# Kernel optimization log

Measured on AMD Instinct MI355X. Metric: run time of the kernel, lower is better.

Reference implementation:

```python
import jax, jax.numpy as jnp
import numpy as np

NUM_USER = 100000
NUM_ITEM = 50000
N = NUM_USER + NUM_ITEM          # total nodes
D = 64                            # dim_latent
E = 2400000                       # nnz of sparse graph
NUM_LAYER = 3


def setup_inputs() -> dict:
    key = jax.random.key(0)
    k1, k2, k3, k4, k5 = jax.random.split(key, 5)
    user_emb = jax.random.normal(k1, (NUM_USER, D), dtype=jnp.float32)
    item_emb = jax.random.normal(k2, (NUM_ITEM, D), dtype=jnp.float32)
    graph_rows = jax.random.randint(k3, (E,), 0, N, dtype=jnp.int32)
    graph_cols = jax.random.randint(k4, (E,), 0, N, dtype=jnp.int32)
    # normalized-adjacency-like small positive values
    graph_vals = jax.random.uniform(k5, (E,), dtype=jnp.float32) * 0.01
    return {
        "user_emb": user_emb,
        "item_emb": item_emb,
        "graph_vals": graph_vals,
        "graph_rows": graph_rows,
        "graph_cols": graph_cols,
    }


def _spmm(vals, rows, cols, x):
    # sparse [N,N] @ dense [N,D] via gather + segment_sum
    gathered = vals[:, None] * x[cols]            # [E, D]
    return jax.ops.segment_sum(gathered, rows, num_segments=N)  # [N, D]


def reference(user_emb, item_emb, graph_vals, graph_rows, graph_cols):
    all_emb = jnp.concatenate([user_emb, item_emb], axis=0)   # [N, D]
    acc = all_emb
    emb = all_emb
    for _ in range(NUM_LAYER):
        emb = _spmm(graph_vals, graph_rows, graph_cols, emb)
        acc = acc + emb
    light_out = acc / jnp.float32(NUM_LAYER + 1)              # mean over layer dim
    return (light_out, user_emb, item_emb)
```

## Files before the change

### kernel.cpp

```cpp
#include <hip/hip_runtime.h>


#define NUM_USER 100000
#define NUM_ITEM 50000
#define NTOT     150000
#define DIM      64
#define NEDGE    2400000
#define ND       (NTOT * DIM)

#define RPB    256
#define NB     586
#define CAP    4736
#define CHUNK  4096
#define NCHUNK 586
#define EPT    16
#define CVTB   1024

typedef float v2f __attribute__((ext_vector_type(2)));

static __device__ __forceinline__ unsigned pk_fp8x4(float a, float b, float c, float d) {
    int p = 0;
    p = __builtin_amdgcn_cvt_pk_fp8_f32(a, b, p, false);
    p = __builtin_amdgcn_cvt_pk_fp8_f32(c, d, p, true);
    return (unsigned)p;
}
static __device__ __forceinline__ unsigned char f2fp8(float a) {
    return (unsigned char)(__builtin_amdgcn_cvt_pk_fp8_f32(a, 0.f, 0, false) & 0xFF);
}
static __device__ __forceinline__ float fp8lo2f(unsigned w) {
    const v2f t = __builtin_amdgcn_cvt_pk_f32_fp8((int)w, false);
    return t[0];
}

__global__ __launch_bounds__(256) void phaseA_kernel(
    const int*   __restrict__ rows,
    const int*   __restrict__ cols,
    const float* __restrict__ vals,
    int*            __restrict__ cursor,
    unsigned*       __restrict__ crG,
    unsigned short* __restrict__ vbG,
    const float*    __restrict__ user,
    const float*    __restrict__ item,
    unsigned*       __restrict__ xq)
{
    __shared__ unsigned       s_cr[CHUNK];
    __shared__ unsigned short s_vb[CHUNK];
    __shared__ unsigned short s_bk[CHUNK];
    __shared__ int s_hist[NB];
    __shared__ int s_scan[NB];
    __shared__ int s_dst[NB];
    __shared__ int s_cur[NB];
    __shared__ int s_part[256];

    if (blockIdx.x >= NCHUNK) {
        const int nvec  = ND / 4;
        const int userv = NUM_USER * DIM / 4;
        for (int i = (blockIdx.x - NCHUNK) * 256 + threadIdx.x; i < nvec;
             i += CVTB * 256) {
            const float4 v = (i < userv) ? ((const float4*)user)[i]
                                         : ((const float4*)item)[i - userv];
            xq[i] = pk_fp8x4(v.x * 16.f, v.y * 16.f, v.z * 16.f, v.w * 16.f);
        }
        return;
    }

    const int t    = threadIdx.x;
    const int base = blockIdx.x * CHUNK;
    const int n    = min(CHUNK, NEDGE - base);

    for (int i = t; i < NB; i += 256) s_hist[i] = 0;
    __syncthreads();

    int            mrow[EPT];
    unsigned       mcol[EPT];
    unsigned short mvb[EPT];
#pragma unroll
    for (int k = 0; k < EPT; ++k) {
        const int i = t + k * 256;
        if (i < n) {
            const int e = base + i;
            mrow[k] = rows[e];
            mcol[k] = (unsigned)cols[e];
            mvb[k]  = f2fp8(vals[e] * 64.f);
            atomicAdd(&s_hist[mrow[k] >> 8], 1);
        } else mrow[k] = -1;
    }
    __syncthreads();

    int loc[3]; int ssum = 0;
#pragma unroll
    for (int k = 0; k < 3; ++k) {
        const int i = t * 3 + k;
        loc[k] = (i < NB) ? s_hist[i] : 0;
        ssum += loc[k];
    }
    s_part[t] = ssum;
    __syncthreads();
    for (int o = 1; o < 256; o <<= 1) {
        const int v = (t >= o) ? s_part[t - o] : 0;
        __syncthreads();
        s_part[t] += v;
        __syncthreads();
    }
    int run = s_part[t] - ssum;
#pragma unroll
    for (int k = 0; k < 3; ++k) {
        const int i = t * 3 + k;
        if (i < NB) { s_scan[i] = run; run += loc[k]; }
    }
    __syncthreads();

    for (int i = t; i < NB; i += 256) {
        const int c = s_hist[i];
        s_dst[i] = i * CAP + (c ? atomicAdd(&cursor[i], c) : 0);
        s_cur[i] = s_scan[i];
    }
    __syncthreads();

#pragma unroll
    for (int k = 0; k < EPT; ++k) {
        if (mrow[k] >= 0) {
            const int b   = mrow[k] >> 8;
            const int pos = atomicAdd(&s_cur[b], 1);
            s_cr[pos] = mcol[k] | ((unsigned)(mrow[k] & 255) << 18);
            s_vb[pos] = mvb[k];
            s_bk[pos] = (unsigned short)b;
        }
    }
    __syncthreads();

    for (int p = t; p < n; p += 256) {
        const int b = s_bk[p];
        const int g = s_dst[b] + (p - s_scan[b]);
        crG[g] = s_cr[p];
        vbG[g] = s_vb[p];
    }
}

__global__ __launch_bounds__(256) void phaseB_kernel(
    const int*      __restrict__ cursor,
    unsigned*       __restrict__ crG,
    unsigned short* __restrict__ vbG,
    int*            __restrict__ rowbeg,
    int*            __restrict__ rowend)
{
    __shared__ unsigned       s_cr[CAP];
    __shared__ unsigned short s_vb[CAP];
    __shared__ unsigned short s_idx[CAP];
    __shared__ int s_hist[RPB];
    __shared__ int s_scan[RPB];
    __shared__ int s_cur[RPB];

    const int b = blockIdx.x, t = threadIdx.x;
    const int gbase = b * CAP;
    const int cnt = cursor[b];

    s_hist[t] = 0;
    __syncthreads();
    for (int p = t; p < cnt; p += 256) {
        const unsigned cr = crG[gbase + p];
        s_cr[p] = cr;
        s_vb[p] = vbG[gbase + p];
        atomicAdd(&s_hist[cr >> 18], 1);
    }
    __syncthreads();

    const int h = s_hist[t];
    s_scan[t] = h;
    __syncthreads();
    for (int o = 1; o < 256; o <<= 1) {
        const int v = (t >= o) ? s_scan[t - o] : 0;
        __syncthreads();
        s_scan[t] += v;
        __syncthreads();
    }
    const int excl = s_scan[t] - h;
    s_cur[t] = excl;
    __syncthreads();

    for (int p = t; p < cnt; p += 256) {
        const int r   = s_cr[p] >> 18;
        const int pos = atomicAdd(&s_cur[r], 1);
        s_idx[pos] = (unsigned short)p;
    }
    __syncthreads();

    for (int p = t; p < cnt; p += 256) {
        const int i = s_idx[p];
        crG[gbase + p] = ((s_cr[i] & 0x3FFFFu) << 8) | (unsigned)(s_vb[i] & 0xFFu);
    }
    const int row = b * RPB + t;
    if (row < NTOT) {
        rowbeg[row] = gbase + excl;
        rowend[row] = gbase + excl + h;
    }
}

template<int MODE>
__global__ __launch_bounds__(256) void spmm_pull(
    const int*            __restrict__ rowbeg,
    const int*            __restrict__ rowend,
    const unsigned*       __restrict__ cv,
    const unsigned char*  __restrict__ xq,
    unsigned*             __restrict__ destq,
    float*                __restrict__ acc,
    const float*          __restrict__ user,
    const float*          __restrict__ item,
    float*                __restrict__ out)
{
    const int r    = (blockIdx.x * 256 + threadIdx.x) >> 6;
    const int lane = threadIdx.x & 63;
    const int g    = lane >> 3;
    const int l    = lane & 7;

    const int beg = __builtin_amdgcn_readfirstlane(rowbeg[r]);
    const int end = __builtin_amdgcn_readfirstlane(rowend[r]);

    v2f a0 = {0.f,0.f}, a1 = {0.f,0.f}, a2 = {0.f,0.f}, a3 = {0.f,0.f};
    for (int k = beg + g; k < end; k += 16) {
        const bool h1 = (k + 8) < end;
        const int  kb = h1 ? k + 8 : k;
        const unsigned ca = cv[k];
        unsigned cb = cv[kb];
        cb = h1 ? cb : (cb & ~0xFFu);

        const float va = fp8lo2f(ca);
        const float vb = fp8lo2f(cb);

        const unsigned offA = ((ca & ~0xFFu) >> 2) + (l << 3);
        const unsigned offB = ((cb & ~0xFFu) >> 2) + (l << 3);
        const uint2 wa = *reinterpret_cast<const uint2*>(xq + offA);
        const uint2 wb = *reinterpret_cast<const uint2*>(xq + offB);

        const v2f va2 = {va, va}, vb2 = {vb, vb};
        a0 += va2 * __builtin_amdgcn_cvt_pk_f32_fp8((int)wa.x, false);
        a1 += va2 * __builtin_amdgcn_cvt_pk_f32_fp8((int)wa.x, true);
        a2 += va2 * __builtin_amdgcn_cvt_pk_f32_fp8((int)wa.y, false);
        a3 += va2 * __builtin_amdgcn_cvt_pk_f32_fp8((int)wa.y, true);
        a0 += vb2 * __builtin_amdgcn_cvt_pk_f32_fp8((int)wb.x, false);
        a1 += vb2 * __builtin_amdgcn_cvt_pk_f32_fp8((int)wb.x, true);
        a2 += vb2 * __builtin_amdgcn_cvt_pk_f32_fp8((int)wb.y, false);
        a3 += vb2 * __builtin_amdgcn_cvt_pk_f32_fp8((int)wb.y, true);
    }

    float f0 = a0[0], f1 = a0[1], f2 = a1[0], f3 = a1[1];
    float f4 = a2[0], f5 = a2[1], f6 = a3[0], f7 = a3[1];
#define RED(x) x += __shfl_xor(x, 8); x += __shfl_xor(x, 16); x += __shfl_xor(x, 32);
    RED(f0) RED(f1) RED(f2) RED(f3) RED(f4) RED(f5) RED(f6) RED(f7)
#undef RED
    const float s = 1.f / 1024.f;
    f0 *= s; f1 *= s; f2 *= s; f3 *= s; f4 *= s; f5 *= s; f6 *= s; f7 *= s;

    if (g == 0) {
        const int o = r * DIM + (l << 3);
        if (MODE == 0) {
            *reinterpret_cast<float4*>(acc + o)     = make_float4(f0, f1, f2, f3);
            *reinterpret_cast<float4*>(acc + o + 4) = make_float4(f4, f5, f6, f7);
        } else if (MODE == 1) {
            float4 x0 = *reinterpret_cast<float4*>(acc + o);
            float4 x1 = *reinterpret_cast<float4*>(acc + o + 4);
            x0.x += f0; x0.y += f1; x0.z += f2; x0.w += f3;
            x1.x += f4; x1.y += f5; x1.z += f6; x1.w += f7;
            *reinterpret_cast<float4*>(acc + o)     = x0;
            *reinterpret_cast<float4*>(acc + o + 4) = x1;
        } else {
            const float* aep = (r < NUM_USER)
                ? user + (size_t)r * DIM + (l << 3)
                : item + (size_t)(r - NUM_USER) * DIM + (l << 3);
            const float4 e0 = *reinterpret_cast<const float4*>(aep);
            const float4 e1 = *reinterpret_cast<const float4*>(aep + 4);
            const float4 x0 = *reinterpret_cast<const float4*>(acc + o);
            const float4 x1 = *reinterpret_cast<const float4*>(acc + o + 4);
            float4 lo0, lo1;
            lo0.x = (x0.x + f0 + e0.x) * 0.25f;
            lo0.y = (x0.y + f1 + e0.y) * 0.25f;
            lo0.z = (x0.z + f2 + e0.z) * 0.25f;
            lo0.w = (x0.w + f3 + e0.w) * 0.25f;
            lo1.x = (x1.x + f4 + e1.x) * 0.25f;
            lo1.y = (x1.y + f5 + e1.y) * 0.25f;
            lo1.z = (x1.z + f6 + e1.z) * 0.25f;
            lo1.w = (x1.w + f7 + e1.w) * 0.25f;
            *reinterpret_cast<float4*>(out + o)          = lo0;
            *reinterpret_cast<float4*>(out + o + 4)      = lo1;
            *reinterpret_cast<float4*>(out + ND + o)     = e0;
            *reinterpret_cast<float4*>(out + ND + o + 4) = e1;
        }
        if (MODE == 0 || MODE == 1) {
            uint2 pk;
            pk.x = pk_fp8x4(f0 * 16.f, f1 * 16.f, f2 * 16.f, f3 * 16.f);
            pk.y = pk_fp8x4(f4 * 16.f, f5 * 16.f, f6 * 16.f, f7 * 16.f);
            *reinterpret_cast<uint2*>(destq + (r << 4) + (l << 1)) = pk;
        }
    }
}


__global__ __launch_bounds__(256) void spmm_atomic(
    const float* __restrict__ vals, const int* __restrict__ rows,
    const int* __restrict__ cols, const float* __restrict__ x0,
    const float* __restrict__ x1, int split, float* __restrict__ out)
{
    const int lane = threadIdx.x & 63;
    const long wave   = ((long)blockIdx.x * blockDim.x + threadIdx.x) >> 6;
    const long nwaves = ((long)gridDim.x * blockDim.x) >> 6;
    for (long e = wave; e < NEDGE; e += nwaves) {
        const int   r = rows[e];
        const int   c = cols[e];
        const float v = vals[e];
        const float xv = (c < split) ? x0[(long)c * DIM + lane]
                                     : x1[(long)(c - split) * DIM + lane];
        atomicAdd(&out[(long)r * DIM + lane], v * xv);
    }
}

__global__ __launch_bounds__(256) void add2_kernel(
    const float* __restrict__ a, const float* __restrict__ b,
    float* __restrict__ acc)
{
    const int nvec = ND / 4;
    for (int i = blockIdx.x * blockDim.x + threadIdx.x; i < nvec;
         i += gridDim.x * blockDim.x) {
        const float4 av = ((const float4*)a)[i];
        const float4 bv = ((const float4*)b)[i];
        float4 o;
        o.x = av.x + bv.x; o.y = av.y + bv.y;
        o.z = av.z + bv.z; o.w = av.w + bv.w;
        ((float4*)acc)[i] = o;
    }
}

__global__ __launch_bounds__(256) void finalize3_kernel(
    const float* __restrict__ user, const float* __restrict__ item,
    float* __restrict__ out)
{
    const int nvec  = ND / 4;
    const int userv = NUM_USER * DIM / 4;
    for (int i = blockIdx.x * blockDim.x + threadIdx.x; i < nvec;
         i += gridDim.x * blockDim.x) {
        const float4 ae = (i < userv) ? ((const float4*)user)[i]
                                      : ((const float4*)item)[i - userv];
        const float4 ac = ((const float4*)out)[i];
        const float4 e3 = ((const float4*)(out + ND))[i];
        float4 lo;
        lo.x = (ae.x + ac.x + e3.x) * 0.25f;
        lo.y = (ae.y + ac.y + e3.y) * 0.25f;
        lo.z = (ae.z + ac.z + e3.z) * 0.25f;
        lo.w = (ae.w + ac.w + e3.w) * 0.25f;
        ((float4*)out)[i] = lo;
        ((float4*)(out + ND))[i] = ae;
    }
}


extern "C" void kernel_launch(void* const* d_in, const int* in_sizes, int n_in,
                              void* d_out, int out_size, void* d_ws, size_t ws_size,
                              hipStream_t stream) {
    const float* user = (const float*)d_in[0];
    const float* item = (const float*)d_in[1];
    const float* vals = (const float*)d_in[2];
    const int*   rows = (const int*)d_in[3];
    const int*   cols = (const int*)d_in[4];

    float* out = (float*)d_out;
    float* acc = out;

    char* w = (char*)d_ws;
    unsigned char* xq0 = (unsigned char*)w;
    unsigned char* xq1 = xq0 + ND;
    unsigned*      crG = (unsigned*)(xq1 + ND);
    int*   rowbeg = (int*)(crG + (size_t)NB * CAP);
    int*   rowend = rowbeg + NTOT;
    int*   cursor = rowend + NTOT;
    unsigned short* vbG = (unsigned short*)(cursor + NB);
    const size_t ws_need = (size_t)ND * 2 + (size_t)NB * CAP * 6
                         + (size_t)(2 * NTOT + NB) * 4 + 64;

    if (ws_size >= ws_need) {
        hipMemsetAsync(cursor, 0, (size_t)NB * 4, stream);
        phaseA_kernel<<<NCHUNK + CVTB, 256, 0, stream>>>(
            rows, cols, vals, cursor, crG, vbG, user, item, (unsigned*)xq0);
        phaseB_kernel<<<NB, 256, 0, stream>>>(cursor, crG, vbG, rowbeg, rowend);

        const int spmm_blocks = NTOT / 4;
        spmm_pull<0><<<spmm_blocks, 256, 0, stream>>>(rowbeg, rowend, crG,
            xq0, (unsigned*)xq1, acc, nullptr, nullptr, nullptr);
        spmm_pull<1><<<spmm_blocks, 256, 0, stream>>>(rowbeg, rowend, crG,
            xq1, (unsigned*)xq0, acc, nullptr, nullptr, nullptr);
        spmm_pull<2><<<spmm_blocks, 256, 0, stream>>>(rowbeg, rowend, crG,
            xq0, nullptr, acc, user, item, out);
    } else {
        float* bufA = (float*)d_ws;
        float* out1 = out + ND;
        const size_t nd_bytes = (size_t)ND * sizeof(float);
        hipMemsetAsync(out1, 0, nd_bytes, stream);
        spmm_atomic<<<2048, 256, 0, stream>>>(vals, rows, cols, user, item, NUM_USER, out1);
        hipMemsetAsync(bufA, 0, nd_bytes, stream);
        spmm_atomic<<<2048, 256, 0, stream>>>(vals, rows, cols, out1, out1, NTOT, bufA);
        add2_kernel<<<2048, 256, 0, stream>>>(out1, bufA, acc);
        hipMemsetAsync(out1, 0, nd_bytes, stream);
        spmm_atomic<<<2048, 256, 0, stream>>>(vals, rows, cols, bufA, bufA, NTOT, out1);
        finalize3_kernel<<<2048, 256, 0, stream>>>(user, item, out);
    }
}
```

Before: 233.6 us.

## Process row cohorts per wave in column-segment order for cache locality

Phase B now sorts edges within each row by a 3-bit column-range key, so every row gets 8 segment ranges. The SpMM kernel assigns 37 consecutive rows to each wave and walks those rows segment by segment. This keeps the gathered fp8 source rows inside a narrow column window at any moment, which is meant to improve L2/MALL hit rates. In exchange each wave holds 37 register accumulators, each lane gathers only 2 bytes per edge, the grid is much smaller, and the loop has more index overhead.

Measured after the change: 740.2 us. +216.8%, slower.

```diff
diff --git a/kernel.cpp b/kernel.cpp
--- a/kernel.cpp
+++ b/kernel.cpp
@@ -16,6 +16,11 @@
 #define EPT    16
 #define CVTB   1024
 
+#define NSEG   5
+#define NKEY   2048
+#define RW     37
+#define COHORT_BLOCKS 1014
+
 typedef float v2f __attribute__((ext_vector_type(2)));
 
 static __device__ __forceinline__ unsigned pk_fp8x4(float a, float b, float c, float d) {
@@ -26,10 +31,6 @@
 }
 static __device__ __forceinline__ unsigned char f2fp8(float a) {
     return (unsigned char)(__builtin_amdgcn_cvt_pk_fp8_f32(a, 0.f, 0, false) & 0xFF);
-}
-static __device__ __forceinline__ float fp8lo2f(unsigned w) {
-    const v2f t = __builtin_amdgcn_cvt_pk_f32_fp8((int)w, false);
-    return t[0];
 }
 
 __global__ __launch_bounds__(256) void phaseA_kernel(
@@ -140,47 +141,56 @@
 __global__ __launch_bounds__(256) void phaseB_kernel(
     const int*      __restrict__ cursor,
     unsigned*       __restrict__ crG,
-    unsigned short* __restrict__ vbG,
-    int*            __restrict__ rowbeg,
-    int*            __restrict__ rowend)
+    const unsigned short* __restrict__ vbG,
+    int2*           __restrict__ segbe)
 {
     __shared__ unsigned       s_cr[CAP];
     __shared__ unsigned short s_vb[CAP];
     __shared__ unsigned short s_idx[CAP];
-    __shared__ int s_hist[RPB];
-    __shared__ int s_scan[RPB];
-    __shared__ int s_cur[RPB];
+    __shared__ int s_hist[NKEY];
+    __shared__ int s_cur[NKEY];
+    __shared__ int s_part[256];
 
     const int b = blockIdx.x, t = threadIdx.x;
     const int gbase = b * CAP;
     const int cnt = cursor[b];
 
-    s_hist[t] = 0;
+    for (int i = t; i < NKEY; i += 256) s_hist[i] = 0;
     __syncthreads();
     for (int p = t; p < cnt; p += 256) {
         const unsigned cr = crG[gbase + p];
         s_cr[p] = cr;
         s_vb[p] = vbG[gbase + p];
-        atomicAdd(&s_hist[cr >> 18], 1);
-    }
-    __syncthreads();
-
-    const int h = s_hist[t];
-    s_scan[t] = h;
+        const int key = (int)(((cr >> 18) << 3) | ((cr >> 15) & 7u));
+        atomicAdd(&s_hist[key], 1);
+    }
+    __syncthreads();
+
+    int loc[8]; int ssum = 0;
+#pragma unroll
+    for (int j = 0; j < 8; ++j) { loc[j] = s_hist[t * 8 + j]; ssum += loc[j]; }
+    s_part[t] = ssum;
     __syncthreads();
     for (int o = 1; o < 256; o <<= 1) {
-        const int v = (t >= o) ? s_scan[t - o] : 0;
+        const int v = (t >= o) ? s_part[t - o] : 0;
         __syncthreads();
-        s_scan[t] += v;
+        s_part[t] += v;
         __syncthreads();
     }
-    const int excl = s_scan[t] - h;
-    s_cur[t] = excl;
+    int run = s_part[t] - ssum;
+    __syncthreads();
+#pragma unroll
+    for (int j = 0; j < 8; ++j) {
+        s_hist[t * 8 + j] = run;
+        s_cur[t * 8 + j]  = run;
+        run += loc[j];
+    }
     __syncthreads();
 
     for (int p = t; p < cnt; p += 256) {
-        const int r   = s_cr[p] >> 18;
-        const int pos = atomicAdd(&s_cur[r], 1);
+        const unsigned cr = s_cr[p];
+        const int key = (int)(((cr >> 18) << 3) | ((cr >> 15) & 7u));
+        const int pos = atomicAdd(&s_cur[key], 1);
         s_idx[pos] = (unsigned short)p;
     }
     __syncthreads();
@@ -189,107 +199,98 @@
         const int i = s_idx[p];
         crG[gbase + p] = ((s_cr[i] & 0x3FFFFu) << 8) | (unsigned)(s_vb[i] & 0xFFu);
     }
-    const int row = b * RPB + t;
-    if (row < NTOT) {
-        rowbeg[row] = gbase + excl;
-        rowend[row] = gbase + excl + h;
+    __syncthreads();
+
+    for (int i = t; i < NKEY; i += 256) {
+        const int row = b * RPB + (i >> 3);
+        if (row < NTOT)
+            segbe[(row << 3) | (i & 7)] =
+                make_int2(gbase + s_hist[i], gbase + s_cur[i]);
     }
 }
 
 template<int MODE>
-__global__ __launch_bounds__(256) void spmm_pull(
-    const int*            __restrict__ rowbeg,
-    const int*            __restrict__ rowend,
+__global__ __launch_bounds__(256, 4) void spmm_cohort(
+    const int2*           __restrict__ segbe,
     const unsigned*       __restrict__ cv,
     const unsigned char*  __restrict__ xq,
-    unsigned*             __restrict__ destq,
+    unsigned char*        __restrict__ destq,
     float*                __restrict__ acc,
     const float*          __restrict__ user,
     const float*          __restrict__ item,
     float*                __restrict__ out)
 {
-    const int r    = (blockIdx.x * 256 + threadIdx.x) >> 6;
+    const int wave = ((blockIdx.x << 8) + threadIdx.x) >> 6;
     const int lane = threadIdx.x & 63;
-    const int g    = lane >> 3;
-    const int l    = lane & 7;
-
-    const int beg = __builtin_amdgcn_readfirstlane(rowbeg[r]);
-    const int end = __builtin_amdgcn_readfirstlane(rowend[r]);
-
-    v2f a0 = {0.f,0.f}, a1 = {0.f,0.f}, a2 = {0.f,0.f}, a3 = {0.f,0.f};
-    for (int k = beg + g; k < end; k += 16) {
-        const bool h1 = (k + 8) < end;
-        const int  kb = h1 ? k + 8 : k;
-        const unsigned ca = cv[k];
-        unsigned cb = cv[kb];
-        cb = h1 ? cb : (cb & ~0xFFu);
-
-        const float va = fp8lo2f(ca);
-        const float vb = fp8lo2f(cb);
-
-        const unsigned offA = ((ca & ~0xFFu) >> 2) + (l << 3);
-        const unsigned offB = ((cb & ~0xFFu) >> 2) + (l << 3);
-        const uint2 wa = *reinterpret_cast<const uint2*>(xq + offA);
-        const uint2 wb = *reinterpret_cast<const uint2*>(xq + offB);
-
-        const v2f va2 = {va, va}, vb2 = {vb, vb};
-        a0 += va2 * __builtin_amdgcn_cvt_pk_f32_fp8((int)wa.x, false);
-        a1 += va2 * __builtin_amdgcn_cvt_pk_f32_fp8((int)wa.x, true);
-        a2 += va2 * __builtin_amdgcn_cvt_pk_f32_fp8((int)wa.y, false);
-        a3 += va2 * __builtin_amdgcn_cvt_pk_f32_fp8((int)wa.y, true);
-        a0 += vb2 * __builtin_amdgcn_cvt_pk_f32_fp8((int)wb.x, false);
-        a1 += vb2 * __builtin_amdgcn_cvt_pk_f32_fp8((int)wb.x, true);
-        a2 += vb2 * __builtin_amdgcn_cvt_pk_f32_fp8((int)wb.y, false);
-        a3 += vb2 * __builtin_amdgcn_cvt_pk_f32_fp8((int)wb.y, true);
-    }
-
-    float f0 = a0[0], f1 = a0[1], f2 = a1[0], f3 = a1[1];
-    float f4 = a2[0], f5 = a2[1], f6 = a3[0], f7 = a3[1];
-#define RED(x) x += __shfl_xor(x, 8); x += __shfl_xor(x, 16); x += __shfl_xor(x, 32);
-    RED(f0) RED(f1) RED(f2) RED(f3) RED(f4) RED(f5) RED(f6) RED(f7)
-#undef RED
-    const float s = 1.f / 1024.f;
-    f0 *= s; f1 *= s; f2 *= s; f3 *= s; f4 *= s; f5 *= s; f6 *= s; f7 *= s;
-
-    if (g == 0) {
-        const int o = r * DIM + (l << 3);
-        if (MODE == 0) {
-            *reinterpret_cast<float4*>(acc + o)     = make_float4(f0, f1, f2, f3);
-            *reinterpret_cast<float4*>(acc + o + 4) = make_float4(f4, f5, f6, f7);
-        } else if (MODE == 1) {
-            float4 x0 = *reinterpret_cast<float4*>(acc + o);
-            float4 x1 = *reinterpret_cast<float4*>(acc + o + 4);
-            x0.x += f0; x0.y += f1; x0.z += f2; x0.w += f3;
-            x1.x += f4; x1.y += f5; x1.z += f6; x1.w += f7;
-            *reinterpret_cast<float4*>(acc + o)     = x0;
-            *reinterpret_cast<float4*>(acc + o + 4) = x1;
-        } else {
-            const float* aep = (r < NUM_USER)
-                ? user + (size_t)r * DIM + (l << 3)
-                : item + (size_t)(r - NUM_USER) * DIM + (l << 3);
-            const float4 e0 = *reinterpret_cast<const float4*>(aep);
-            const float4 e1 = *reinterpret_cast<const float4*>(aep + 4);
-            const float4 x0 = *reinterpret_cast<const float4*>(acc + o);
-            const float4 x1 = *reinterpret_cast<const float4*>(acc + o + 4);
-            float4 lo0, lo1;
-            lo0.x = (x0.x + f0 + e0.x) * 0.25f;
-            lo0.y = (x0.y + f1 + e0.y) * 0.25f;
-            lo0.z = (x0.z + f2 + e0.z) * 0.25f;
-            lo0.w = (x0.w + f3 + e0.w) * 0.25f;
-            lo1.x = (x1.x + f4 + e1.x) * 0.25f;
-            lo1.y = (x1.y + f5 + e1.y) * 0.25f;
-            lo1.z = (x1.z + f6 + e1.z) * 0.25f;
-            lo1.w = (x1.w + f7 + e1.w) * 0.25f;
-            *reinterpret_cast<float4*>(out + o)          = lo0;
-            *reinterpret_cast<float4*>(out + o + 4)      = lo1;
-            *reinterpret_cast<float4*>(out + ND + o)     = e0;
-            *reinterpret_cast<float4*>(out + ND + o + 4) = e1;
+    const int g    = lane >> 5;
+    const int l2   = (lane & 31) << 1;
+    const int r0   = wave * RW;
+
+    v2f a[RW];
+#pragma unroll
+    for (int i = 0; i < RW; ++i) a[i] = (v2f){0.f, 0.f};
+
+    for (int s = 0; s < NSEG; ++s) {
+#pragma unroll
+        for (int i = 0; i < RW; ++i) {
+            const int r = r0 + i;
+            if (r < NTOT) {
+                const int2 be = segbe[(r << 3) | s];
+                for (int k = be.x; k < be.y; k += 4) {
+                    const int kend = be.y - 1;
+                    const int ka = k + g;
+                    const int kb = k + 2 + g;
+                    unsigned ca = cv[min(ka, kend)];
+                    unsigned cb = cv[min(kb, kend)];
+                    if (ka > kend) ca = 0u;
+                    if (kb > kend) cb = 0u;
+                    const v2f va = __builtin_amdgcn_cvt_pk_f32_fp8((int)ca, false);
+                    const v2f vb = __builtin_amdgcn_cvt_pk_f32_fp8((int)cb, false);
+                    const unsigned offa = ((ca & 0xFFFFFF00u) >> 2) + l2;
+                    const unsigned offb = ((cb & 0xFFFFFF00u) >> 2) + l2;
+                    const unsigned short wa = *(const unsigned short*)(xq + offa);
+                    const unsigned short wb = *(const unsigned short*)(xq + offb);
+                    const v2f xa = __builtin_amdgcn_cvt_pk_f32_fp8((int)(unsigned)wa, false);
+                    const v2f xb = __builtin_amdgcn_cvt_pk_f32_fp8((int)(unsigned)wb, false);
+                    a[i] += (v2f){va[0], va[0]} * xa;
+                    a[i] += (v2f){vb[0], vb[0]} * xb;
+                }
+            }
         }
-        if (MODE == 0 || MODE == 1) {
-            uint2 pk;
-            pk.x = pk_fp8x4(f0 * 16.f, f1 * 16.f, f2 * 16.f, f3 * 16.f);
-            pk.y = pk_fp8x4(f4 * 16.f, f5 * 16.f, f6 * 16.f, f7 * 16.f);
-            *reinterpret_cast<uint2*>(destq + (r << 4) + (l << 1)) = pk;
+    }
+
+    const float sc = 1.f / 1024.f;
+#pragma unroll
+    for (int i = 0; i < RW; ++i) {
+        const int r = r0 + i;
+        if (r >= NTOT) continue;
+        float f0 = a[i][0], f1 = a[i][1];
+        f0 += __shfl_xor(f0, 32);
+        f1 += __shfl_xor(f1, 32);
+        f0 *= sc; f1 *= sc;
+        if (lane < 32) {
+            const int o = (r << 6) + l2;
+            if (MODE == 0) {
+                *(float2*)(acc + o) = make_float2(f0, f1);
+            } else if (MODE == 1) {
+                float2 tch = *(float2*)(acc + o);
+                tch.x += f0; tch.y += f1;
+                *(float2*)(acc + o) = tch;
+            } else {
+                const float* aep = (r < NUM_USER)
+                    ? user + ((size_t)r << 6) + l2
+                    : item + ((size_t)(r - NUM_USER) << 6) + l2;
+                const float2 ae = *(const float2*)aep;
+                const float2 tch = *(const float2*)(acc + o);
+                *(float2*)(out + o) =
+                    make_float2((tch.x + f0 + ae.x) * 0.25f,
+                                (tch.y + f1 + ae.y) * 0.25f);
+                *(float2*)(out + ND + o) = ae;
+            }
+            if (MODE != 2) {
+                const unsigned p = pk_fp8x4(f0 * 16.f, f1 * 16.f, 0.f, 0.f);
+                *(unsigned short*)(destq + o) = (unsigned short)(p & 0xFFFFu);
+            }
         }
     }
 }
@@ -368,25 +369,23 @@
     unsigned char* xq0 = (unsigned char*)w;
     unsigned char* xq1 = xq0 + ND;
     unsigned*      crG = (unsigned*)(xq1 + ND);
-    int*   rowbeg = (int*)(crG + (size_t)NB * CAP);
-    int*   rowend = rowbeg + NTOT;
-    int*   cursor = rowend + NTOT;
-    unsigned short* vbG = (unsigned short*)(cursor + NB);
+    unsigned short* vbG = (unsigned short*)(crG + (size_t)NB * CAP);
+    int2*  segbe  = (int2*)(vbG + (size_t)NB * CAP);
+    int*   cursor = (int*)(segbe + (size_t)NTOT * 8);
     const size_t ws_need = (size_t)ND * 2 + (size_t)NB * CAP * 6
-                         + (size_t)(2 * NTOT + NB) * 4 + 64;
+                         + (size_t)NTOT * 8 * 8 + (size_t)NB * 4 + 64;
 
     if (ws_size >= ws_need) {
         hipMemsetAsync(cursor, 0, (size_t)NB * 4, stream);
         phaseA_kernel<<<NCHUNK + CVTB, 256, 0, stream>>>(
             rows, cols, vals, cursor, crG, vbG, user, item, (unsigned*)xq0);
-        phaseB_kernel<<<NB, 256, 0, stream>>>(cursor, crG, vbG, rowbeg, rowend);
-
-        const int spmm_blocks = NTOT / 4;
-        spmm_pull<0><<<spmm_blocks, 256, 0, stream>>>(rowbeg, rowend, crG,
-            xq0, (unsigned*)xq1, acc, nullptr, nullptr, nullptr);
-        spmm_pull<1><<<spmm_blocks, 256, 0, stream>>>(rowbeg, rowend, crG,
-            xq1, (unsigned*)xq0, acc, nullptr, nullptr, nullptr);
-        spmm_pull<2><<<spmm_blocks, 256, 0, stream>>>(rowbeg, rowend, crG,
+        phaseB_kernel<<<NB, 256, 0, stream>>>(cursor, crG, vbG, segbe);
+
+        spmm_cohort<0><<<COHORT_BLOCKS, 256, 0, stream>>>(segbe, crG,
+            xq0, xq1, acc, nullptr, nullptr, nullptr);
+        spmm_cohort<1><<<COHORT_BLOCKS, 256, 0, stream>>>(segbe, crG,
+            xq1, xq0, acc, nullptr, nullptr, nullptr);
+        spmm_cohort<2><<<COHORT_BLOCKS, 256, 0, stream>>>(segbe, crG,
             xq0, nullptr, acc, user, item, out);
     } else {
         float* bufA = (float*)d_ws;
```

## Split fp8 embedding into two column halves and run SpMM per half

Applied to the files above, without the earlier changes.

Stores the fp8-quantized embedding as two separate 32-column halves, each a contiguous block, and launches each SpMM layer twice, once per half. Each half-pass gathers 4 bytes per lane instead of 8, so the randomly gathered working set per pass halves (4.8 MB) and may fit better in cache. In exchange, the CSR index stream and row pointers are read twice per layer and the kernel launch count doubles.

Measured after the change: 336.4 us. 44.0% more time.

```diff
diff --git a/kernel.cpp b/kernel.cpp
--- a/kernel.cpp
+++ b/kernel.cpp
@@ -7,6 +7,7 @@
 #define DIM      64
 #define NEDGE    2400000
 #define ND       (NTOT * DIM)
+#define HWORDS   (NTOT * 8)
 
 #define RPB    256
 #define NB     586
@@ -59,7 +60,9 @@
              i += CVTB * 256) {
             const float4 v = (i < userv) ? ((const float4*)user)[i]
                                          : ((const float4*)item)[i - userv];
-            xq[i] = pk_fp8x4(v.x * 16.f, v.y * 16.f, v.z * 16.f, v.w * 16.f);
+            const int row = i >> 4, h = (i >> 3) & 1, j = i & 7;
+            xq[h * HWORDS + row * 8 + j] =
+                pk_fp8x4(v.x * 16.f, v.y * 16.f, v.z * 16.f, v.w * 16.f);
         }
         return;
     }
@@ -140,7 +143,7 @@
 __global__ __launch_bounds__(256) void phaseB_kernel(
     const int*      __restrict__ cursor,
     unsigned*       __restrict__ crG,
-    unsigned short* __restrict__ vbG,
+    const unsigned short* __restrict__ vbG,
     int*            __restrict__ rowbeg,
     int*            __restrict__ rowend)
 {
@@ -196,7 +199,7 @@
     }
 }
 
-template<int MODE>
+template<int MODE, int H>
 __global__ __launch_bounds__(256) void spmm_pull(
     const int*            __restrict__ rowbeg,
     const int*            __restrict__ rowend,
@@ -216,7 +219,9 @@
     const int beg = __builtin_amdgcn_readfirstlane(rowbeg[r]);
     const int end = __builtin_amdgcn_readfirstlane(rowend[r]);
 
-    v2f a0 = {0.f,0.f}, a1 = {0.f,0.f}, a2 = {0.f,0.f}, a3 = {0.f,0.f};
+    const unsigned char* xh = xq + (size_t)H * (HWORDS * 4);
+
+    v2f a0 = {0.f,0.f}, a1 = {0.f,0.f};
     for (int k = beg + g; k < end; k += 16) {
         const bool h1 = (k + 8) < end;
         const int  kb = h1 ? k + 8 : k;
@@ -227,69 +232,50 @@
         const float va = fp8lo2f(ca);
         const float vb = fp8lo2f(cb);
 
-        const unsigned offA = ((ca & ~0xFFu) >> 2) + (l << 3);
-        const unsigned offB = ((cb & ~0xFFu) >> 2) + (l << 3);
-        const uint2 wa = *reinterpret_cast<const uint2*>(xq + offA);
-        const uint2 wb = *reinterpret_cast<const uint2*>(xq + offB);
+        const unsigned offA = ((ca & 0xFFFFFF00u) >> 3) + (l << 2);
+        const unsigned offB = ((cb & 0xFFFFFF00u) >> 3) + (l << 2);
+        const unsigned wa = *reinterpret_cast<const unsigned*>(xh + offA);
+        const unsigned wb = *reinterpret_cast<const unsigned*>(xh + offB);
 
         const v2f va2 = {va, va}, vb2 = {vb, vb};
-        a0 += va2 * __builtin_amdgcn_cvt_pk_f32_fp8((int)wa.x, false);
-        a1 += va2 * __builtin_amdgcn_cvt_pk_f32_fp8((int)wa.x, true);
-        a2 += va2 * __builtin_amdgcn_cvt_pk_f32_fp8((int)wa.y, false);
-        a3 += va2 * __builtin_amdgcn_cvt_pk_f32_fp8((int)wa.y, true);
-        a0 += vb2 * __builtin_amdgcn_cvt_pk_f32_fp8((int)wb.x, false);
-        a1 += vb2 * __builtin_amdgcn_cvt_pk_f32_fp8((int)wb.x, true);
-        a2 += vb2 * __builtin_amdgcn_cvt_pk_f32_fp8((int)wb.y, false);
-        a3 += vb2 * __builtin_amdgcn_cvt_pk_f32_fp8((int)wb.y, true);
+        a0 += va2 * __builtin_amdgcn_cvt_pk_f32_fp8((int)wa, false);
+        a1 += va2 * __builtin_amdgcn_cvt_pk_f32_fp8((int)wa, true);
+        a0 += vb2 * __builtin_amdgcn_cvt_pk_f32_fp8((int)wb, false);
+        a1 += vb2 * __builtin_amdgcn_cvt_pk_f32_fp8((int)wb, true);
     }
 
     float f0 = a0[0], f1 = a0[1], f2 = a1[0], f3 = a1[1];
-    float f4 = a2[0], f5 = a2[1], f6 = a3[0], f7 = a3[1];
 #define RED(x) x += __shfl_xor(x, 8); x += __shfl_xor(x, 16); x += __shfl_xor(x, 32);
-    RED(f0) RED(f1) RED(f2) RED(f3) RED(f4) RED(f5) RED(f6) RED(f7)
+    RED(f0) RED(f1) RED(f2) RED(f3)
 #undef RED
     const float s = 1.f / 1024.f;
-    f0 *= s; f1 *= s; f2 *= s; f3 *= s; f4 *= s; f5 *= s; f6 *= s; f7 *= s;
+    f0 *= s; f1 *= s; f2 *= s; f3 *= s;
 
     if (g == 0) {
-        const int o = r * DIM + (l << 3);
+        const int o = (r << 6) + (H << 5) + (l << 2);
         if (MODE == 0) {
-            *reinterpret_cast<float4*>(acc + o)     = make_float4(f0, f1, f2, f3);
-            *reinterpret_cast<float4*>(acc + o + 4) = make_float4(f4, f5, f6, f7);
+            *reinterpret_cast<float4*>(acc + o) = make_float4(f0, f1, f2, f3);
         } else if (MODE == 1) {
             float4 x0 = *reinterpret_cast<float4*>(acc + o);
-            float4 x1 = *reinterpret_cast<float4*>(acc + o + 4);
             x0.x += f0; x0.y += f1; x0.z += f2; x0.w += f3;
-            x1.x += f4; x1.y += f5; x1.z += f6; x1.w += f7;
-            *reinterpret_cast<float4*>(acc + o)     = x0;
-            *reinterpret_cast<float4*>(acc + o + 4) = x1;
+            *reinterpret_cast<float4*>(acc + o) = x0;
         } else {
             const float* aep = (r < NUM_USER)
-                ? user + (size_t)r * DIM + (l << 3)
-                : item + (size_t)(r - NUM_USER) * DIM + (l << 3);
-            const float4 e0 = *reinterpret_cast<const float4*>(aep);
-            const float4 e1 = *reinterpret_cast<const float4*>(aep + 4);
+                ? user + ((size_t)r << 6) + (H << 5) + (l << 2)
+                : item + ((size_t)(r - NUM_USER) << 6) + (H << 5) + (l << 2);
+            const float4 ae = *reinterpret_cast<const float4*>(aep);
             const float4 x0 = *reinterpret_cast<const float4*>(acc + o);
-            const float4 x1 = *reinterpret_cast<const float4*>(acc + o + 4);
-            float4 lo0, lo1;
-            lo0.x = (x0.x + f0 + e0.x) * 0.25f;
-            lo0.y = (x0.y + f1 + e0.y) * 0.25f;
-            lo0.z = (x0.z + f2 + e0.z) * 0.25f;
-            lo0.w = (x0.w + f3 + e0.w) * 0.25f;
-            lo1.x = (x1.x + f4 + e1.x) * 0.25f;
-            lo1.y = (x1.y + f5 + e1.y) * 0.25f;
-            lo1.z = (x1.z + f6 + e1.z) * 0.25f;
-            lo1.w = (x1.w + f7 + e1.w) * 0.25f;
-            *reinterpret_cast<float4*>(out + o)          = lo0;
-            *reinterpret_cast<float4*>(out + o + 4)      = lo1;
-            *reinterpret_cast<float4*>(out + ND + o)     = e0;
-            *reinterpret_cast<float4*>(out + ND + o + 4) = e1;
+            float4 lo;
+            lo.x = (x0.x + f0 + ae.x) * 0.25f;
+            lo.y = (x0.y + f1 + ae.y) * 0.25f;
+            lo.z = (x0.z + f2 + ae.z) * 0.25f;
+            lo.w = (x0.w + f3 + ae.w) * 0.25f;
+            *reinterpret_cast<float4*>(out + o)      = lo;
+            *reinterpret_cast<float4*>(out + ND + o) = ae;
         }
         if (MODE == 0 || MODE == 1) {
-            uint2 pk;
-            pk.x = pk_fp8x4(f0 * 16.f, f1 * 16.f, f2 * 16.f, f3 * 16.f);
-            pk.y = pk_fp8x4(f4 * 16.f, f5 * 16.f, f6 * 16.f, f7 * 16.f);
-            *reinterpret_cast<uint2*>(destq + (r << 4) + (l << 1)) = pk;
+            destq[H * HWORDS + (r << 3) + l] =
+                pk_fp8x4(f0 * 16.f, f1 * 16.f, f2 * 16.f, f3 * 16.f);
         }
     }
 }
@@ -382,11 +368,17 @@
         phaseB_kernel<<<NB, 256, 0, stream>>>(cursor, crG, vbG, rowbeg, rowend);
 
         const int spmm_blocks = NTOT / 4;
-        spmm_pull<0><<<spmm_blocks, 256, 0, stream>>>(rowbeg, rowend, crG,
+        spmm_pull<0,0><<<spmm_blocks, 256, 0, stream>>>(rowbeg, rowend, crG,
             xq0, (unsigned*)xq1, acc, nullptr, nullptr, nullptr);
-        spmm_pull<1><<<spmm_blocks, 256, 0, stream>>>(rowbeg, rowend, crG,
+        spmm_pull<0,1><<<spmm_blocks, 256, 0, stream>>>(rowbeg, rowend, crG,
+            xq0, (unsigned*)xq1, acc, nullptr, nullptr, nullptr);
+        spmm_pull<1,0><<<spmm_blocks, 256, 0, stream>>>(rowbeg, rowend, crG,
             xq1, (unsigned*)xq0, acc, nullptr, nullptr, nullptr);
-        spmm_pull<2><<<spmm_blocks, 256, 0, stream>>>(rowbeg, rowend, crG,
+        spmm_pull<1,1><<<spmm_blocks, 256, 0, stream>>>(rowbeg, rowend, crG,
+            xq1, (unsigned*)xq0, acc, nullptr, nullptr, nullptr);
+        spmm_pull<2,0><<<spmm_blocks, 256, 0, stream>>>(rowbeg, rowend, crG,
+            xq0, nullptr, acc, user, item, out);
+        spmm_pull<2,1><<<spmm_blocks, 256, 0, stream>>>(rowbeg, rowend, crG,
             xq0, nullptr, acc, user, item, out);
     } else {
         float* bufA = (float*)d_ws;
```
